# Kernel optimization log

Hardware: AMD Instinct MI355X
Metric: run time of the kernel (lower is better)

## Reference

```python
import jax, jax.numpy as jnp
import numpy as np


def setup_inputs() -> dict:
    key = jax.random.key(0)
    k0, k1, k2, k3, k4 = jax.random.split(key, 5)
    n, c, s, h, w = 4, 128, 31, 32, 22
    x = jax.random.normal(k0, (n, c, s, h, w), dtype=jnp.float32)
    # 1x1 conv to a single channel == per-pixel dot over channels + scalar bias
    scale = 1.0 / np.sqrt(c).astype(np.float32)
    w1 = jax.random.normal(k1, (c,), dtype=jnp.float32) * scale
    b1 = jax.random.normal(k2, (), dtype=jnp.float32) * 0.01
    w2 = jax.random.normal(k3, (c,), dtype=jnp.float32) * scale
    b2 = jax.random.normal(k4, (), dtype=jnp.float32) * 0.01
    return {"x": x, "w1": w1, "b1": b1, "w2": w2, "b2": b2, "top_k": 16}


def reference(x, w1, b1, w2, b2, top_k):
    n, c, s, h, w = x.shape
    hw = h * w
    ns = n * (s - 1)
    # adjacent-frame pairs; 1x1 conv (C->1) as channel contraction
    X0 = jnp.einsum('ncshw,c->nshw', x[:, :, : s - 1], w1) + b1  # (n, s-1, h, w)
    X1 = jnp.einsum('ncshw,c->nshw', x[:, :, 1:], w2) + b2       # (n, s-1, h, w)
    X0 = X0.reshape(ns, hw)
    X1 = X1.reshape(ns, hw)
    # outer-product scores per frame pair, softmax over last dim
    attention = jax.nn.softmax(X0[:, :, None] * X1[:, None, :], axis=2)  # (ns, hw, hw)
    # top-k values along last dim -> (ns, hw, k); torch .view(ns, k, h, w)
    # is a raw row-major reinterpretation, so a plain reshape is faithful.
    vals, _ = jax.lax.top_k(attention, top_k)
    vals = vals.reshape(n, s - 1, top_k, h, w)
    # trans_out: (n, s-1, k, h, w) -> (n, k, s-1, h, w)
    return jnp.transpose(vals, (0, 2, 1, 3, 4))
```

## Files before the change

### kernel.cpp

```cpp
#include <hip/hip_runtime.h>
#include <math.h>

#define NB   4
#define C    128
#define S    31
#define HW   704
#define T    30
#define NS   120
#define K    16

__global__ __launch_bounds__(256) void conv_kernel(
    const float* __restrict__ x,
    const float* __restrict__ w1, const float* __restrict__ b1p,
    const float* __restrict__ w2, const float* __restrict__ b2p,
    float* __restrict__ A, float* __restrict__ B) {
  const int tid   = threadIdx.x;
  const int chunk = blockIdx.x % 11;
  const int fr    = blockIdx.x / 11;
  const int sf    = fr % S;
  const int n     = fr / S;
  const int p     = chunk * 64 + (tid & 63);
  const int cg    = tid >> 6;

  const float* xp = x + (((size_t)(n * C + cg * 32) * S + sf) * HW) + p;
  const float* wA = w1 + cg * 32;
  const float* wB = w2 + cg * 32;
  float acc1 = 0.f, acc2 = 0.f;
#pragma unroll
  for (int c = 0; c < 32; ++c) {
    float xv = xp[(size_t)c * (S * HW)];
    acc1 = fmaf(xv, wA[c], acc1);
    acc2 = fmaf(xv, wB[c], acc2);
  }
  __shared__ float s1[256], s2[256];
  s1[tid] = acc1;
  s2[tid] = acc2;
  __syncthreads();
  if (tid < 64) {
    float a1 = (s1[tid] + s1[tid + 64]) + (s1[tid + 128] + s1[tid + 192]);
    float a2 = (s2[tid] + s2[tid + 64]) + (s2[tid + 128] + s2[tid + 192]);
    if (sf < T)  A[(n * T + sf) * HW + p]       = a1 + b1p[0];
    if (sf >= 1) B[(n * T + (sf - 1)) * HW + p] = a2 + b2p[0];
  }
}

__global__ __launch_bounds__(512) void sort_kernel(
    const float* __restrict__ B,
    float* __restrict__ btop, float* __restrict__ bbot) {
  __shared__ float s[1024];
  const int i   = blockIdx.x;
  const int tid = threadIdx.x;
  const float* bi = B + i * HW;
  for (int q = tid; q < 1024; q += 512)
    s[q] = (q < HW) ? bi[q] : INFINITY;
  __syncthreads();
#pragma unroll 1
  for (int k = 2; k <= 1024; k <<= 1) {
#pragma unroll 1
    for (int j = k >> 1; j > 0; j >>= 1) {
#pragma unroll
      for (int idx = tid; idx < 1024; idx += 512) {
        int ixj = idx ^ j;
        if (ixj > idx) {
          float a = s[idx], b = s[ixj];
          if ((a > b) == ((idx & k) == 0)) { s[idx] = b; s[ixj] = a; }
        }
      }
      __syncthreads();
    }
  }
  if (tid < K) {
    bbot[i * K + tid] = s[tid];
    btop[i * K + tid] = s[HW - 1 - tid];
  }
}

__global__ __launch_bounds__(256) void softmax_topk_kernel(
    const float* __restrict__ A, const float* __restrict__ B,
    const float* __restrict__ btop, const float* __restrict__ bbot,
    float* __restrict__ out) {
  const int lane = threadIdx.x & 63;
  const int R    = blockIdx.x * 4 + (threadIdx.x >> 6);
  const int i    = R / HW;
  const int r    = R % HW;

  const float av  = A[R];
  const float st0 = btop[i * K];
  const float sb0 = bbot[i * K];
  const float m   = (av >= 0.f) ? av * st0 : av * sb0;
  const float L2E   = 1.4426950408889634f;
  const float av2   = av * L2E;
  const float negm2 = -m * L2E;

  const float* __restrict__ bi = B + i * HW;
  float part = 0.f;
#pragma unroll
  for (int j = 0; j < 11; ++j) {
    part += exp2f(fmaf(av2, bi[j * 64 + lane], negm2));
  }
#pragma unroll
  for (int off = 1; off < 64; off <<= 1)
    part += __shfl_xor(part, off, 64);
  const float inv = 1.0f / part;

  if (lane < K) {
    const float sel = (av >= 0.f) ? btop[i * K + lane] : bbot[i * K + lane];
    const float val = exp2f(fmaf(av2, sel, negm2)) * inv;
    const int n  = i / T;
    const int t  = i % T;
    const int jo = r / 44;
    const int po = (r % 44) * K;
    out[((((size_t)n * K + jo) * T) + t) * HW + po + lane] = val;
  }
}

extern "C" void kernel_launch(void* const* d_in, const int* in_sizes, int n_in,
                              void* d_out, int out_size, void* d_ws, size_t ws_size,
                              hipStream_t stream) {
  (void)in_sizes; (void)n_in; (void)out_size; (void)ws_size;
  const float* x  = (const float*)d_in[0];
  const float* w1 = (const float*)d_in[1];
  const float* b1 = (const float*)d_in[2];
  const float* w2 = (const float*)d_in[3];
  const float* b2 = (const float*)d_in[4];
  float* out = (float*)d_out;

  float* A    = (float*)d_ws;
  float* B    = A + NS * HW;
  float* btop = B + NS * HW;
  float* bbot = btop + NS * K;

  conv_kernel<<<124 * 11, 256, 0, stream>>>(x, w1, b1, w2, b2, A, B);
  sort_kernel<<<NS, 512, 0, stream>>>(B, btop, bbot);
  softmax_topk_kernel<<<(NS * HW) / 4, 256, 0, stream>>>(A, B, btop, bbot, out);
}
```

Measured before the change: 127.5 us.

## Fuse bitonic sort and softmax top-k into one per-frame kernel

Merges the sort kernel and the softmax/top-k kernel so that each frame-pair block sorts B and then computes the softmax denominators and top-k values itself. A and B are staged in shared memory, and the top/bottom 16 values stay in LDS instead of going through global memory. Each wave processes 4 rows at once to increase ILP, and the exp calls use the native exp2 builtin. This removes one kernel launch and the repeated global/L2 reads of B. The cost is that the softmax phase now runs on only 120 blocks, which may leave much of the GPU idle.

```diff
diff --git a/kernel.cpp b/kernel.cpp
--- a/kernel.cpp
+++ b/kernel.cpp
@@ -44,16 +44,24 @@
   }
 }
 
-__global__ __launch_bounds__(512) void sort_kernel(
-    const float* __restrict__ B,
-    float* __restrict__ btop, float* __restrict__ bbot) {
+__global__ __launch_bounds__(512) void sort_softmax_kernel(
+    const float* __restrict__ A, const float* __restrict__ B,
+    float* __restrict__ out) {
   __shared__ float s[1024];
+  __shared__ float sB[HW];
+  __shared__ float sA[HW];
+  __shared__ float stp[K], sbt[K];
   const int i   = blockIdx.x;
   const int tid = threadIdx.x;
   const float* bi = B + i * HW;
-  for (int q = tid; q < 1024; q += 512)
-    s[q] = (q < HW) ? bi[q] : INFINITY;
+  const float* ai = A + i * HW;
+  for (int q = tid; q < 1024; q += 512) {
+    float v = (q < HW) ? bi[q] : INFINITY;
+    s[q] = v;
+    if (q < HW) { sB[q] = v; sA[q] = ai[q]; }
+  }
   __syncthreads();
+
 #pragma unroll 1
   for (int k = 2; k <= 1024; k <<= 1) {
 #pragma unroll 1
@@ -70,47 +78,52 @@
     }
   }
   if (tid < K) {
-    bbot[i * K + tid] = s[tid];
-    btop[i * K + tid] = s[HW - 1 - tid];
+    sbt[tid] = s[tid];
+    stp[tid] = s[HW - 1 - tid];
   }
-}
+  __syncthreads();
 
-__global__ __launch_bounds__(256) void softmax_topk_kernel(
-    const float* __restrict__ A, const float* __restrict__ B,
-    const float* __restrict__ btop, const float* __restrict__ bbot,
-    float* __restrict__ out) {
-  const int lane = threadIdx.x & 63;
-  const int R    = blockIdx.x * 4 + (threadIdx.x >> 6);
-  const int i    = R / HW;
-  const int r    = R % HW;
+  const int lane = tid & 63;
+  const int wv   = tid >> 6;
+  const float L2E = 1.4426950408889634f;
+  const float t0  = stp[0], b0 = sbt[0];
+  const int   n   = i / T;
+  const int   t   = i % T;
+  float* obase = out + (((size_t)n * K) * T + t) * HW;
 
-  const float av  = A[R];
-  const float st0 = btop[i * K];
-  const float sb0 = bbot[i * K];
-  const float m   = (av >= 0.f) ? av * st0 : av * sb0;
-  const float L2E   = 1.4426950408889634f;
-  const float av2   = av * L2E;
-  const float negm2 = -m * L2E;
-
-  const float* __restrict__ bi = B + i * HW;
-  float part = 0.f;
+#pragma unroll 1
+  for (int g = 0; g < 22; ++g) {
+    const int r0 = wv * 88 + g * 4;
+    float av[4], a2[4], nm[4], part[4];
 #pragma unroll
-  for (int j = 0; j < 11; ++j) {
-    part += exp2f(fmaf(av2, bi[j * 64 + lane], negm2));
-  }
+    for (int u = 0; u < 4; ++u) {
+      av[u]   = sA[r0 + u];
+      a2[u]   = av[u] * L2E;
+      nm[u]   = -((av[u] >= 0.f) ? av[u] * t0 : av[u] * b0) * L2E;
+      part[u] = 0.f;
+    }
 #pragma unroll
-  for (int off = 1; off < 64; off <<= 1)
-    part += __shfl_xor(part, off, 64);
-  const float inv = 1.0f / part;
-
-  if (lane < K) {
-    const float sel = (av >= 0.f) ? btop[i * K + lane] : bbot[i * K + lane];
-    const float val = exp2f(fmaf(av2, sel, negm2)) * inv;
-    const int n  = i / T;
-    const int t  = i % T;
-    const int jo = r / 44;
-    const int po = (r % 44) * K;
-    out[((((size_t)n * K + jo) * T) + t) * HW + po + lane] = val;
+    for (int j = 0; j < 11; ++j) {
+      float bv = sB[j * 64 + lane];
+#pragma unroll
+      for (int u = 0; u < 4; ++u)
+        part[u] += __builtin_amdgcn_exp2f(fmaf(a2[u], bv, nm[u]));
+    }
+#pragma unroll
+    for (int off = 1; off < 64; off <<= 1) {
+#pragma unroll
+      for (int u = 0; u < 4; ++u)
+        part[u] += __shfl_xor(part[u], off, 64);
+    }
+    if (lane < K) {
+#pragma unroll
+      for (int u = 0; u < 4; ++u) {
+        const int r   = r0 + u;
+        const float sel = (av[u] >= 0.f) ? stp[lane] : sbt[lane];
+        const float val = __builtin_amdgcn_exp2f(fmaf(a2[u], sel, nm[u])) / part[u];
+        obase[(size_t)(r / 44) * (T * HW) + (r % 44) * K + lane] = val;
+      }
+    }
   }
 }
 
@@ -125,12 +138,9 @@
   const float* b2 = (const float*)d_in[4];
   float* out = (float*)d_out;
 
-  float* A    = (float*)d_ws;
-  float* B    = A + NS * HW;
-  float* btop = B + NS * HW;
-  float* bbot = btop + NS * K;
+  float* A = (float*)d_ws;
+  float* B = A + NS * HW;
 
   conv_kernel<<<124 * 11, 256, 0, stream>>>(x, w1, b1, w2, b2, A, B);
-  sort_kernel<<<NS, 512, 0, stream>>>(B, btop, bbot);
-  softmax_topk_kernel<<<(NS * HW) / 4, 256, 0, stream>>>(A, B, btop, bbot, out);
+  sort_softmax_kernel<<<NS, 512, 0, stream>>>(A, B, out);
 }
```

Result: slower. 132.2 us (+3.7%).
